# Optimization experiments

Hardware: AMD Instinct MI355X
Metric: run time of the kernel (lower is better)

The kernel has to match this reference:

```python
import jax, jax.numpy as jnp
import numpy as np

V, E, H, ENC, ATT = 10000, 256, 512, 512, 512
B, S, NF, MAXLEN = 128, 25, 196, 64


def setup_inputs() -> dict:
    key = jax.random.key(0)
    ks = jax.random.split(key, 24)
    g = lambda k, shp: (jax.random.normal(k, shp, dtype=jnp.float32) * 0.05)
    emb = g(ks[0], (V, E)).at[0].set(0.0)  # padding_idx=0 row zeroed
    return {
        'decoder_input': jax.random.randint(ks[1], (B, S), 0, V, dtype=jnp.int32),
        'encoder_outputs': jax.random.normal(ks[2], (B, NF, ENC), dtype=jnp.float32),
        'emb': emb,
        'pos_emb': g(ks[3], (MAXLEN, E)),
        'Uw': g(ks[4], (ATT, ENC)), 'Ub': g(ks[5], (ATT,)),
        'Ww': g(ks[6], (ATT, H)), 'Wb': g(ks[7], (ATT,)),
        'Aw': g(ks[8], (1, ATT)), 'Ab': g(ks[9], (1,)),
        'init_h_w': g(ks[10], (H, ENC)), 'init_h_b': g(ks[11], (H,)),
        'init_c_w': g(ks[12], (H, ENC)), 'init_c_b': g(ks[13], (H,)),
        'W_ih': g(ks[14], (4 * H, E + ENC)), 'W_hh': g(ks[15], (4 * H, H)),
        'b_ih': g(ks[16], (4 * H,)), 'b_hh': g(ks[17], (4 * H,)),
        'fcn_w': g(ks[18], (V, H)), 'fcn_b': g(ks[19], (V,)),
    }


def reference(decoder_input, encoder_outputs, emb, pos_emb, Uw, Ub, Ww, Wb, Aw, Ab,
              init_h_w, init_h_b, init_c_w, init_c_b, W_ih, W_hh, b_ih, b_hh,
              fcn_w, fcn_b):
    # Loop-invariant attention key projection: U(features) -> [B, NF, ATT]
    u_hs = jnp.einsum('bne,ae->bna', encoder_outputs, Uw) + Ub
    mean_enc = encoder_outputs.mean(axis=1)                  # [B, ENC]
    h0 = mean_enc @ init_h_w.T + init_h_b                    # [B, H]
    c0 = mean_enc @ init_c_w.T + init_c_b
    tokens = decoder_input.T                                 # [S, B]
    positions = jnp.arange(tokens.shape[0])

    def step(carry, inp):
        h, c = carry
        tok, pos = inp
        embeds = emb[tok] + pos_emb[pos]                     # [B, E]
        w_ah = h @ Ww.T + Wb                                 # [B, ATT]
        scores = jnp.tanh(u_hs + w_ah[:, None, :]) @ Aw[0] + Ab[0]  # [B, NF]
        alpha = jax.nn.softmax(scores, axis=1)
        context = jnp.einsum('bnd,bn->bd', encoder_outputs, alpha)  # [B, ENC]
        x = jnp.concatenate([embeds, context], axis=1)       # [B, E+ENC]
        gates = x @ W_ih.T + b_ih + h @ W_hh.T + b_hh        # [B, 4H]
        i, f, g_, o = jnp.split(gates, 4, axis=1)
        c_new = jax.nn.sigmoid(f) * c + jax.nn.sigmoid(i) * jnp.tanh(g_)
        h_new = jax.nn.sigmoid(o) * jnp.tanh(c_new)
        out = h_new @ fcn_w.T + fcn_b                        # [B, V] (dropout=eval identity)
        return (h_new, c_new), (out, alpha)

    _, (outs, alphas) = jax.lax.scan(step, (h0, c0), (tokens, positions))
    return outs.transpose(1, 0, 2), alphas.transpose(1, 0, 2)
```

## Files before the change

### kernel.cpp

```cpp
#include <hip/hip_runtime.h>

constexpr int B_ = 128, S_ = 25, NF_ = 196, ENC_ = 512, ATT_ = 512;
constexpr int H_ = 512, E_ = 256, V_ = 10000, G4_ = 2048;
constexpr int VPAD_ = 10112;

typedef __attribute__((ext_vector_type(8))) __bf16 bf16x8;
typedef __attribute__((ext_vector_type(4))) __bf16 bf16x4;
typedef __attribute__((ext_vector_type(4))) float f32x4;

__device__ __forceinline__ float bflo(unsigned u) {
    return __builtin_bit_cast(float, u << 16);
}
__device__ __forceinline__ float bfhi(unsigned u) {
    return __builtin_bit_cast(float, u & 0xffff0000u);
}
__device__ __forceinline__ float fast_tanhf(float x) {
    x = fminf(fmaxf(x, -15.f), 15.f);
    return 1.f - 2.f * __fdividef(1.f, __expf(2.f * x) + 1.f);
}
__device__ __forceinline__ float fast_sigf(float x) {
    x = fminf(fmaxf(x, -30.f), 30.f);
    return __fdividef(1.f, 1.f + __expf(-x));
}

__device__ __forceinline__ int gperm(int n) {
    int j = (n & 15) + ((n >> 6) << 4);
    int g = (n >> 4) & 3;
    return g * 512 + j;
}

__global__ __launch_bounds__(256) void k_setup(
    const float* __restrict__ enc, __bf16* __restrict__ enc_bf,
    const float* __restrict__ Uw, __bf16* __restrict__ Uw_bf,
    const float* __restrict__ Ww, unsigned* __restrict__ W2,
    const float* __restrict__ W_ih, __bf16* __restrict__ WihE_r,
    const float* __restrict__ W_hh, __bf16* __restrict__ Wcat,
    const float* __restrict__ b_ih, const float* __restrict__ b_hh,
    float* __restrict__ bsum_r,
    const int* __restrict__ dec, const float* __restrict__ emb,
    const float* __restrict__ pose, __bf16* __restrict__ embeds_bf,
    const float* __restrict__ fcw, __bf16* __restrict__ fcw_bf) {
    __shared__ float Ts[32][65];
    int bid = blockIdx.x, t = threadIdx.x;

    if (bid < 12544) {
        int i = bid * 256 + t;
        if (i < 3211264) {
            float4 v = *(const float4*)&enc[(size_t)i * 4];
            bf16x4 o;
            o[0] = (__bf16)v.x; o[1] = (__bf16)v.y; o[2] = (__bf16)v.z; o[3] = (__bf16)v.w;
            *(bf16x4*)&enc_bf[(size_t)i * 4] = o;
        }
    } else if (bid < 12800) {
        int i = (bid - 12544) * 256 + t;
        float4 v = *(const float4*)&Uw[(size_t)i * 4];
        bf16x4 o;
        o[0] = (__bf16)v.x; o[1] = (__bf16)v.y; o[2] = (__bf16)v.z; o[3] = (__bf16)v.w;
        *(bf16x4*)&Uw_bf[(size_t)i * 4] = o;
    } else if (bid < 12928) {
        int l = bid - 12800;
        int k0 = (l & 15) * 32, j0 = (l >> 4) * 64;
        int c = t & 31, rr = t >> 5;
#pragma unroll
        for (int i = 0; i < 8; ++i) {
            int j = j0 + rr + i * 8;
            Ts[c][rr + i * 8] = Ww[(size_t)j * 512 + k0 + c];
        }
        __syncthreads();
#pragma unroll
        for (int i = 0; i < 4; ++i) {
            int kr = (t >> 5) + i * 8;
            int jc = t & 31;
            __bf16 b0 = (__bf16)Ts[kr][2 * jc], b1 = (__bf16)Ts[kr][2 * jc + 1];
            unsigned u = (unsigned)__builtin_bit_cast(unsigned short, b0)
                       | ((unsigned)__builtin_bit_cast(unsigned short, b1) << 16);
            W2[(size_t)(k0 + kr) * 256 + (j0 >> 1) + jc] = u;
        }
    } else if (bid < 14976) {
        int n = bid - 12928;
        int row = gperm(n);
        WihE_r[(size_t)n * 256 + t] = (__bf16)W_ih[(size_t)row * 768 + t];
    } else if (bid < 17024) {
        int n = bid - 14976;
        int row = gperm(n);
#pragma unroll
        for (int i = 0; i < 4; ++i) {
            int k = t + i * 256;
            float v = (k < 512) ? W_ih[(size_t)row * 768 + 256 + k]
                                : W_hh[(size_t)row * 512 + (k - 512)];
            Wcat[(size_t)n * 1024 + k] = (__bf16)v;
        }
    } else if (bid < 17032) {
        int n = (bid - 17024) * 256 + t;
        int row = gperm(n);
        bsum_r[n] = b_ih[row] + b_hh[row];
    } else if (bid < 20232) {
        int bx = bid - 17032;
        int s = bx >> 7, b = bx & 127;
        int tok = dec[b * S_ + s];
        embeds_bf[(size_t)bx * E_ + t] = (__bf16)(emb[tok * E_ + t] + pose[s * E_ + t]);
    } else {
        int i = (bid - 20232) * 256 + t;
        if (i < VPAD_ * 512 / 4) {
            int e = i * 4;
            int row = e >> 9;
            bf16x4 o;
            if (row < V_) {
                float4 v = *(const float4*)&fcw[(size_t)row * 512 + (e & 511)];
                o[0] = (__bf16)v.x; o[1] = (__bf16)v.y; o[2] = (__bf16)v.z; o[3] = (__bf16)v.w;
            } else {
                o[0] = o[1] = o[2] = o[3] = (__bf16)0.f;
            }
            *(bf16x4*)&fcw_bf[(size_t)e] = o;
        }
    }
}

__global__ __launch_bounds__(1024) void k_init2(const float* __restrict__ enc,
                                                const float* __restrict__ ihw, const float* __restrict__ ihb,
                                                const float* __restrict__ icw, const float* __restrict__ icb,
                                                __bf16* __restrict__ Abuf0, float* __restrict__ cbuf) {
    __shared__ float pm[1024];
    __shared__ __align__(16) float mean[512];
    int b = blockIdx.x, t = threadIdx.x;
    int d = t & 511, q = t >> 9;
    const float* ep = enc + ((size_t)b * 196 + q * 98) * 512 + d;
    float sum = 0.f;
#pragma unroll 7
    for (int n = 0; n < 98; ++n) sum += ep[(size_t)n * 512];
    pm[t] = sum;
    __syncthreads();
    if (t < 512) mean[t] = (pm[t] + pm[t + 512]) * (1.f / 196.f);
    __syncthreads();
    int w = t >> 6, ln = t & 63;
    float4 m4a = *(const float4*)&mean[ln * 8];
    float4 m4b = *(const float4*)&mean[ln * 8 + 4];
#pragma unroll 4
    for (int i = 0; i < 32; ++i) {
        int j = i * 16 + w;
        const float4* wh = (const float4*)&ihw[(size_t)j * 512 + ln * 8];
        const float4* wc = (const float4*)&icw[(size_t)j * 512 + ln * 8];
        float4 ha = wh[0], hb = wh[1], ca = wc[0], cb = wc[1];
        float ah = m4a.x * ha.x + m4a.y * ha.y + m4a.z * ha.z + m4a.w * ha.w
                 + m4b.x * hb.x + m4b.y * hb.y + m4b.z * hb.z + m4b.w * hb.w;
        float ac = m4a.x * ca.x + m4a.y * ca.y + m4a.z * ca.z + m4a.w * ca.w
                 + m4b.x * cb.x + m4b.y * cb.y + m4b.z * cb.z + m4b.w * cb.w;
#pragma unroll
        for (int off = 32; off; off >>= 1) {
            ah += __shfl_xor(ah, off);
            ac += __shfl_xor(ac, off);
        }
        if (ln == 0) {
            Abuf0[(size_t)b * 1024 + 512 + j] = (__bf16)(ah + ihb[j]);
            cbuf[b * 512 + j] = ac + icb[j];
        }
    }
}

__global__ __launch_bounds__(256) void k_gemms(
    const __bf16* __restrict__ Aa, const __bf16* __restrict__ Ba,
    const float* __restrict__ ba, __bf16* __restrict__ Ca,
    const __bf16* __restrict__ Ab, const __bf16* __restrict__ Bb,
    const float* __restrict__ bb, __bf16* __restrict__ Cb) {
    __shared__ __align__(16) __bf16 As[128 * 64];
    __shared__ __align__(16) __bf16 Bs[128 * 64];
    int bid = blockIdx.x, tid = threadIdx.x;
    const __bf16 *A, *Bm;
    const float* bias;
    __bf16* C;
    int lda, K, ldc, m0, n0;
    if (bid < 784) {
        A = Aa; Bm = Ba; bias = ba; C = Ca; lda = 512; K = 512; ldc = 512;
        m0 = (bid % 196) * 128; n0 = (bid / 196) * 128;
    } else {
        int i = bid - 784;
        A = Ab; Bm = Bb; bias = bb; C = Cb; lda = 256; K = 256; ldc = 2048;
        m0 = (i % 25) * 128; n0 = (i / 25) * 128;
    }
    int lane = tid & 63, w = tid >> 6;
    int wm = (w & 1) * 64, wn = (w >> 1) * 64;
    f32x4 acc[4][4] = {};
    int srow = tid >> 3;
    int ke = (tid & 7) * 8;
    int kgw = tid & 7;

    for (int k0 = 0; k0 < K; k0 += 64) {
#pragma unroll
        for (int it = 0; it < 4; ++it) {
            int row = it * 32 + srow;
            bf16x8 av = *(const bf16x8*)(A + (size_t)(m0 + row) * lda + k0 + ke);
            bf16x8 bv = *(const bf16x8*)(Bm + (size_t)(n0 + row) * K + k0 + ke);
            int kg = kgw ^ (row & 7);
            *(bf16x8*)&As[row * 64 + kg * 8] = av;
            *(bf16x8*)&Bs[row * 64 + kg * 8] = bv;
        }
        __syncthreads();
        bf16x8 af[4][2], bfr[4][2];
#pragma unroll
        for (int f = 0; f < 4; ++f) {
#pragma unroll
            for (int ks = 0; ks < 2; ++ks) {
                int ra = wm + f * 16 + (lane & 15);
                int rb = wn + f * 16 + (lane & 15);
                int kgl = ks * 4 + (lane >> 4);
                af[f][ks]  = *(const bf16x8*)&As[ra * 64 + (kgl ^ (ra & 7)) * 8];
                bfr[f][ks] = *(const bf16x8*)&Bs[rb * 64 + (kgl ^ (rb & 7)) * 8];
            }
        }
#pragma unroll
        for (int fm = 0; fm < 4; ++fm)
#pragma unroll
            for (int fn = 0; fn < 4; ++fn)
#pragma unroll
                for (int ks = 0; ks < 2; ++ks)
                    acc[fm][fn] = __builtin_amdgcn_mfma_f32_16x16x32_bf16(
                        af[fm][ks], bfr[fn][ks], acc[fm][fn], 0, 0, 0);
        __syncthreads();
    }
    int cm = (lane >> 4) * 4, cn = lane & 15;
#pragma unroll
    for (int fm = 0; fm < 4; ++fm)
#pragma unroll
        for (int fn = 0; fn < 4; ++fn)
#pragma unroll
            for (int r = 0; r < 4; ++r) {
                int gm = m0 + wm + fm * 16 + cm + r;
                int gn = n0 + wn + fn * 16 + cn;
                C[(size_t)gm * ldc + gn] = (__bf16)(acc[fm][fn][r] + bias[gn]);
            }
}

__global__ __launch_bounds__(256) void k_fcn(
    const __bf16* __restrict__ A, const __bf16* __restrict__ Bm,
    const float* __restrict__ bias1, float* __restrict__ Cout) {
    __shared__ __align__(16) __bf16 As[128 * 64];
    __shared__ __align__(16) __bf16 Bs[128 * 64];
    int tid = threadIdx.x;
    int lane = tid & 63, w = tid >> 6;
    int nwg = gridDim.x * gridDim.y;
    int bid = blockIdx.y * gridDim.x + blockIdx.x;
    int q = nwg >> 3, r0 = nwg & 7;
    int xcd = bid & 7, lid = bid >> 3;
    int wgid = (xcd < r0) ? xcd * (q + 1) + lid : r0 * (q + 1) + (xcd - r0) * q + lid;
    int m0 = (wgid % gridDim.x) * 128;
    int n0 = (wgid / gridDim.x) * 128;

    int wm = (w & 1) * 64, wn = (w >> 1) * 64;
    f32x4 acc[4][4] = {};
    int srow = tid >> 3;
    int ke = (tid & 7) * 8;
    int kgw = tid & 7;

    for (int k0 = 0; k0 < 512; k0 += 64) {
#pragma unroll
        for (int it = 0; it < 4; ++it) {
            int row = it * 32 + srow;
            bf16x8 av = *(const bf16x8*)(A + (size_t)(m0 + row) * 512 + k0 + ke);
            bf16x8 bv = *(const bf16x8*)(Bm + (size_t)(n0 + row) * 512 + k0 + ke);
            int kg = kgw ^ (row & 7);
            *(bf16x8*)&As[row * 64 + kg * 8] = av;
            *(bf16x8*)&Bs[row * 64 + kg * 8] = bv;
        }
        __syncthreads();
        bf16x8 af[4][2], bfr[4][2];
#pragma unroll
        for (int f = 0; f < 4; ++f) {
#pragma unroll
            for (int ks = 0; ks < 2; ++ks) {
                int ra = wm + f * 16 + (lane & 15);
                int rb = wn + f * 16 + (lane & 15);
                int kgl = ks * 4 + (lane >> 4);
                af[f][ks]  = *(const bf16x8*)&As[ra * 64 + (kgl ^ (ra & 7)) * 8];
                bfr[f][ks] = *(const bf16x8*)&Bs[rb * 64 + (kgl ^ (rb & 7)) * 8];
            }
        }
#pragma unroll
        for (int fm = 0; fm < 4; ++fm)
#pragma unroll
            for (int fn = 0; fn < 4; ++fn)
#pragma unroll
                for (int ks = 0; ks < 2; ++ks)
                    acc[fm][fn] = __builtin_amdgcn_mfma_f32_16x16x32_bf16(
                        af[fm][ks], bfr[fn][ks], acc[fm][fn], 0, 0, 0);
        __syncthreads();
    }
    float* LDSf = (float*)As;
    int cm = (lane >> 4) * 4, cn = lane & 15;
#pragma unroll
    for (int c = 0; c < 4; ++c) {
        if ((w & 1) == (c >> 1)) {
            int fmb = (c & 1) * 2;
#pragma unroll
            for (int fi = 0; fi < 2; ++fi) {
                int fm = fmb + fi;
#pragma unroll
                for (int fn = 0; fn < 4; ++fn)
#pragma unroll
                    for (int r = 0; r < 4; ++r)
                        LDSf[(fi * 16 + cm + r) * 128 + wn + fn * 16 + cn] = acc[fm][fn][r];
            }
        }
        __syncthreads();
        int row = tid >> 3, cb = (tid & 7) * 16;
        int grow = m0 + c * 32 + row;
        int orow = (grow & 127) * S_ + (grow >> 7);
        float* dst = Cout + (size_t)orow * V_;
#pragma unroll
        for (int qq = 0; qq < 4; ++qq) {
            int gn = n0 + cb + qq * 4;
            float4 v;
            v.x = LDSf[row * 128 + cb + qq * 4 + 0] + ((gn + 0 < V_) ? bias1[gn + 0] : 0.f);
            v.y = LDSf[row * 128 + cb + qq * 4 + 1] + ((gn + 1 < V_) ? bias1[gn + 1] : 0.f);
            v.z = LDSf[row * 128 + cb + qq * 4 + 2] + ((gn + 2 < V_) ? bias1[gn + 2] : 0.f);
            v.w = LDSf[row * 128 + cb + qq * 4 + 3] + ((gn + 3 < V_) ? bias1[gn + 3] : 0.f);
            if (gn + 3 < V_) {
                *(float4*)&dst[gn] = v;
            } else {
                if (gn + 0 < V_) dst[gn + 0] = v.x;
                if (gn + 1 < V_) dst[gn + 1] = v.y;
                if (gn + 2 < V_) dst[gn + 2] = v.z;
            }
        }
        __syncthreads();
    }
}

__global__ __launch_bounds__(1024) void k_attn2(
    const __bf16* __restrict__ u_hs,
    const unsigned* __restrict__ enc2,
    const unsigned* __restrict__ W2,
    const float* __restrict__ Wb, const float* __restrict__ Aw,
    __bf16* __restrict__ Abuf,
    float* __restrict__ alphas, int s) {
    __shared__ __align__(16) float hs[512];
    __shared__ float wah[512];
    __shared__ float pc[2048];
    __shared__ float sc[200];
    int b = blockIdx.x, t = threadIdx.x;
    int ln = t & 63, w = t >> 6;

    if (t < 256) {
        unsigned u = ((const unsigned*)Abuf)[b * 512 + 256 + t];
        hs[2 * t] = bflo(u); hs[2 * t + 1] = bfhi(u);
    }
    __syncthreads();
    {
        int jp = t & 255, kq = t >> 8;
        float a0 = 0.f, a1 = 0.f;
        const unsigned* wp = W2 + (size_t)(kq * 128) * 256 + jp;
        const float4* h4 = (const float4*)(hs + kq * 128);
#pragma unroll 4
        for (int k4 = 0; k4 < 32; ++k4) {
            float4 hk = h4[k4];
            unsigned w0 = wp[(k4 * 4 + 0) * 256];
            unsigned w1 = wp[(k4 * 4 + 1) * 256];
            unsigned w2 = wp[(k4 * 4 + 2) * 256];
            unsigned w3 = wp[(k4 * 4 + 3) * 256];
            a0 += hk.x * bflo(w0); a1 += hk.x * bfhi(w0);
            a0 += hk.y * bflo(w1); a1 += hk.y * bfhi(w1);
            a0 += hk.z * bflo(w2); a1 += hk.z * bfhi(w2);
            a0 += hk.w * bflo(w3); a1 += hk.w * bfhi(w3);
        }
        pc[kq * 512 + 2 * jp] = a0;
        pc[kq * 512 + 2 * jp + 1] = a1;
    }
    __syncthreads();
    if (t < 512)
        wah[t] = pc[t] + pc[512 + t] + pc[1024 + t] + pc[1536 + t] + Wb[t];
    __syncthreads();
    {
        float av[8], wv[8];
#pragma unroll
        for (int i = 0; i < 8; ++i) { av[i] = Aw[ln * 8 + i]; wv[i] = wah[ln * 8 + i]; }
        for (int n = w; n < NF_; n += 16) {
            bf16x8 u8 = *(const bf16x8*)(u_hs + ((size_t)(b * NF_ + n)) * 512 + ln * 8);
            float acc = 0.f;
#pragma unroll
            for (int i = 0; i < 8; ++i)
                acc += fast_tanhf((float)u8[i] + wv[i]) * av[i];
#pragma unroll
            for (int off = 32; off; off >>= 1) acc += __shfl_xor(acc, off);
            if (ln == 0) sc[n] = __expf(acc);
        }
    }
    __syncthreads();
    float sum = sc[ln] + sc[ln + 64] + sc[ln + 128];
    if (ln < 4) sum += sc[ln + 192];
#pragma unroll
    for (int off = 32; off; off >>= 1) sum += __shfl_xor(sum, off);
    float inv = __fdividef(1.f, sum);
    if (t < NF_) alphas[((size_t)b * S_ + s) * NF_ + t] = sc[t] * inv;
    {
        int p2 = t & 255, q2 = t >> 8;
        float c0 = 0.f, c1 = 0.f;
        for (int i = q2; i < NF_; i += 4) {
            unsigned u = enc2[((size_t)(b * NF_ + i)) * 256 + p2];
            float a = sc[i];
            c0 += a * bflo(u); c1 += a * bfhi(u);
        }
        pc[q2 * 512 + 2 * p2] = c0;
        pc[q2 * 512 + 2 * p2 + 1] = c1;
    }
    __syncthreads();
    if (t < 512)
        Abuf[(size_t)b * 1024 + t] =
            (__bf16)((pc[t] + pc[512 + t] + pc[1024 + t] + pc[1536 + t]) * inv);
}

__global__ __launch_bounds__(256) void k_gates(
    const __bf16* __restrict__ Abuf,
    const __bf16* __restrict__ Wcat,
    const __bf16* __restrict__ gatespre,
    float* __restrict__ cbuf,
    __bf16* __restrict__ AbufN,
    __bf16* __restrict__ Hall_bf,
    int s) {
    __shared__ __align__(16) __bf16 As[2][32 * 64];
    __shared__ __align__(16) __bf16 Bs[2][64 * 64];
    __shared__ float Red[2048];
    int tid = threadIdx.x;
    int lane = tid & 63, w = tid >> 6;
    int m0 = blockIdx.x * 32, n0 = blockIdx.y * 64;
    int kh = w >> 1, wm = (w & 1) * 16;
    f32x4 acc[4] = {};
    int srow = tid >> 3;
    int ke = (tid & 7) * 8;
    int kgw = tid & 7;

    for (int k0 = 0; k0 < 512; k0 += 64) {
#pragma unroll
        for (int h = 0; h < 2; ++h) {
            int kb = h * 512 + k0;
            bf16x8 av = *(const bf16x8*)(Abuf + (size_t)(m0 + srow) * 1024 + kb + ke);
            int kg = kgw ^ (srow & 7);
            *(bf16x8*)&As[h][srow * 64 + kg * 8] = av;
#pragma unroll
            for (int it = 0; it < 2; ++it) {
                int row = it * 32 + srow;
                bf16x8 bv = *(const bf16x8*)(Wcat + (size_t)(n0 + row) * 1024 + kb + ke);
                int kg2 = kgw ^ (row & 7);
                *(bf16x8*)&Bs[h][row * 64 + kg2 * 8] = bv;
            }
        }
        __syncthreads();
        bf16x8 af[2], bfr[4][2];
#pragma unroll
        for (int ks = 0; ks < 2; ++ks) {
            int ra = wm + (lane & 15);
            int kgl = ks * 4 + (lane >> 4);
            af[ks] = *(const bf16x8*)&As[kh][ra * 64 + ((kgl ^ (ra & 7))) * 8];
#pragma unroll
            for (int fn = 0; fn < 4; ++fn) {
                int rb = fn * 16 + (lane & 15);
                bfr[fn][ks] = *(const bf16x8*)&Bs[kh][rb * 64 + ((kgl ^ (rb & 7))) * 8];
            }
        }
#pragma unroll
        for (int fn = 0; fn < 4; ++fn)
#pragma unroll
            for (int ks = 0; ks < 2; ++ks)
                acc[fn] = __builtin_amdgcn_mfma_f32_16x16x32_bf16(
                    af[ks], bfr[fn][ks], acc[fn], 0, 0, 0);
        __syncthreads();
    }
    int base = ((w & 1) * 64 + lane) * 16;
    if (kh == 1) {
#pragma unroll
        for (int fn = 0; fn < 4; ++fn)
#pragma unroll
            for (int r = 0; r < 4; ++r) Red[base + fn * 4 + r] = acc[fn][r];
    }
    __syncthreads();
    if (kh == 0) {
#pragma unroll
        for (int fn = 0; fn < 4; ++fn)
#pragma unroll
            for (int r = 0; r < 4; ++r) acc[fn][r] += Red[base + fn * 4 + r];
        int cm = (lane >> 4) * 4, cn = lane & 15;
        int j = (n0 >> 6) * 16 + cn;
#pragma unroll
        for (int r = 0; r < 4; ++r) {
            int b = m0 + wm + cm + r;
            const __bf16* gp = gatespre + ((size_t)(s * B_ + b)) * G4_ + n0 + cn;
            float qi = acc[0][r] + (float)gp[0];
            float qf = acc[1][r] + (float)gp[16];
            float qg = acc[2][r] + (float)gp[32];
            float qo = acc[3][r] + (float)gp[48];
            float ig = fast_sigf(qi), fg = fast_sigf(qf);
            float gg = fast_tanhf(qg), og = fast_sigf(qo);
            int ci = b * 512 + j;
            float cnew = fg * cbuf[ci] + ig * gg;
            float hn = og * fast_tanhf(cnew);
            cbuf[ci] = cnew;
            __bf16 hb = (__bf16)hn;
            AbufN[(size_t)b * 1024 + 512 + j] = hb;
            Hall_bf[(size_t)(s + 1) * 65536 + ci] = hb;
        }
    }
}

extern "C" void kernel_launch(void* const* d_in, const int* in_sizes, int n_in,
                              void* d_out, int out_size, void* d_ws, size_t ws_size,
                              hipStream_t stream) {
    const int*   dec  = (const int*)d_in[0];
    const float* enc  = (const float*)d_in[1];
    const float* emb  = (const float*)d_in[2];
    const float* pose = (const float*)d_in[3];
    const float* Uw   = (const float*)d_in[4];
    const float* Ub   = (const float*)d_in[5];
    const float* Ww   = (const float*)d_in[6];
    const float* Wb   = (const float*)d_in[7];
    const float* Aw   = (const float*)d_in[8];
    const float* ihw  = (const float*)d_in[10];
    const float* ihb  = (const float*)d_in[11];
    const float* icw  = (const float*)d_in[12];
    const float* icb  = (const float*)d_in[13];
    const float* W_ih = (const float*)d_in[14];
    const float* W_hh = (const float*)d_in[15];
    const float* b_ih = (const float*)d_in[16];
    const float* b_hh = (const float*)d_in[17];
    const float* fcw  = (const float*)d_in[18];
    const float* fcb  = (const float*)d_in[19];
    float* out = (float*)d_out;
    char*  wsb = (char*)d_ws;

    size_t o = 0;
    __bf16*   enc_bf   = (__bf16*)(wsb + o); o += (size_t)25088 * 512 * 2;
    __bf16*   u_hs_bf  = (__bf16*)(wsb + o); o += (size_t)25088 * 512 * 2;
    __bf16*   gpre_bf  = (__bf16*)(wsb + o); o += (size_t)3200 * 2048 * 2;
    __bf16*   Hall_bf  = (__bf16*)(wsb + o); o += (size_t)26 * 65536 * 2;
    float*    cbuf     = (float*)(wsb + o);  o += (size_t)65536 * 4;
    __bf16*   Abuf     = (__bf16*)(wsb + o); o += (size_t)2 * 128 * 1024 * 2;
    __bf16*   Uw_bf    = (__bf16*)(wsb + o); o += (size_t)262144 * 2;
    unsigned* W2       = (unsigned*)(wsb + o); o += (size_t)512 * 256 * 4;
    __bf16*   WihE_r   = (__bf16*)(wsb + o); o += (size_t)2048 * 256 * 2;
    __bf16*   embeds_bf= (__bf16*)(wsb + o); o += (size_t)3200 * 256 * 2;
    __bf16*   Wcat     = (__bf16*)(wsb + o); o += (size_t)2048 * 1024 * 2;
    float*    bsum_r   = (float*)(wsb + o);  o += (size_t)2048 * 4;
    __bf16*   fcw_bf   = (__bf16*)(wsb + o); o += (size_t)VPAD_ * 512 * 2;

    k_setup<<<25288, 256, 0, stream>>>(enc, enc_bf, Uw, Uw_bf, Ww, W2,
                                       W_ih, WihE_r, W_hh, Wcat,
                                       b_ih, b_hh, bsum_r,
                                       dec, emb, pose, embeds_bf, fcw, fcw_bf);
    k_init2<<<B_, 1024, 0, stream>>>(enc, ihw, ihb, icw, icb, Abuf, cbuf);
    k_gemms<<<1184, 256, 0, stream>>>(enc_bf, Uw_bf, Ub, u_hs_bf,
                                      embeds_bf, WihE_r, bsum_r, gpre_bf);

    for (int s = 0; s < S_; ++s) {
        __bf16* Ap = Abuf + (size_t)(s & 1) * 131072;
        __bf16* An = Abuf + (size_t)((s + 1) & 1) * 131072;
        k_attn2<<<B_, 1024, 0, stream>>>(u_hs_bf, (const unsigned*)enc_bf, W2, Wb, Aw,
                                         Ap, out + 32000000, s);
        k_gates<<<dim3(4, 32), 256, 0, stream>>>(Ap, Wcat, gpre_bf, cbuf, An, Hall_bf, s);
    }

    k_fcn<<<dim3(25, 79), 256, 0, stream>>>(Hall_bf + 65536, fcw_bf, fcb, out);
}
```

Measured before the change: 1.410 ms.

## Split gates GEMM into smaller tiles, write fcn output directly, drop activation clamps

```diff
diff --git a/kernel.cpp b/kernel.cpp
--- a/kernel.cpp
+++ b/kernel.cpp
@@ -15,11 +15,10 @@
     return __builtin_bit_cast(float, u & 0xffff0000u);
 }
 __device__ __forceinline__ float fast_tanhf(float x) {
-    x = fminf(fmaxf(x, -15.f), 15.f);
-    return 1.f - 2.f * __fdividef(1.f, __expf(2.f * x) + 1.f);
+    float e = __expf(2.f * x);
+    return 1.f - 2.f * __fdividef(1.f, e + 1.f);
 }
 __device__ __forceinline__ float fast_sigf(float x) {
-    x = fminf(fmaxf(x, -30.f), 30.f);
     return __fdividef(1.f, 1.f + __expf(-x));
 }
 
@@ -284,44 +283,21 @@
                         af[fm][ks], bfr[fn][ks], acc[fm][fn], 0, 0, 0);
         __syncthreads();
     }
-    float* LDSf = (float*)As;
     int cm = (lane >> 4) * 4, cn = lane & 15;
 #pragma unroll
-    for (int c = 0; c < 4; ++c) {
-        if ((w & 1) == (c >> 1)) {
-            int fmb = (c & 1) * 2;
-#pragma unroll
-            for (int fi = 0; fi < 2; ++fi) {
-                int fm = fmb + fi;
-#pragma unroll
-                for (int fn = 0; fn < 4; ++fn)
-#pragma unroll
-                    for (int r = 0; r < 4; ++r)
-                        LDSf[(fi * 16 + cm + r) * 128 + wn + fn * 16 + cn] = acc[fm][fn][r];
-            }
-        }
-        __syncthreads();
-        int row = tid >> 3, cb = (tid & 7) * 16;
-        int grow = m0 + c * 32 + row;
-        int orow = (grow & 127) * S_ + (grow >> 7);
-        float* dst = Cout + (size_t)orow * V_;
-#pragma unroll
-        for (int qq = 0; qq < 4; ++qq) {
-            int gn = n0 + cb + qq * 4;
-            float4 v;
-            v.x = LDSf[row * 128 + cb + qq * 4 + 0] + ((gn + 0 < V_) ? bias1[gn + 0] : 0.f);
-            v.y = LDSf[row * 128 + cb + qq * 4 + 1] + ((gn + 1 < V_) ? bias1[gn + 1] : 0.f);
-            v.z = LDSf[row * 128 + cb + qq * 4 + 2] + ((gn + 2 < V_) ? bias1[gn + 2] : 0.f);
-            v.w = LDSf[row * 128 + cb + qq * 4 + 3] + ((gn + 3 < V_) ? bias1[gn + 3] : 0.f);
-            if (gn + 3 < V_) {
-                *(float4*)&dst[gn] = v;
-            } else {
-                if (gn + 0 < V_) dst[gn + 0] = v.x;
-                if (gn + 1 < V_) dst[gn + 1] = v.y;
-                if (gn + 2 < V_) dst[gn + 2] = v.z;
-            }
-        }
-        __syncthreads();
+    for (int fm = 0; fm < 4; ++fm) {
+#pragma unroll
+        for (int fn = 0; fn < 4; ++fn) {
+#pragma unroll
+            for (int r = 0; r < 4; ++r) {
+                int gm = m0 + wm + fm * 16 + cm + r;
+                int gn = n0 + wn + fn * 16 + cn;
+                if (gn < V_) {
+                    int orow = (gm & 127) * S_ + (gm >> 7);
+                    Cout[(size_t)orow * V_ + gn] = acc[fm][fn][r] + bias1[gn];
+                }
+            }
+        }
     }
 }
 
@@ -415,87 +391,95 @@
     __bf16* __restrict__ AbufN,
     __bf16* __restrict__ Hall_bf,
     int s) {
-    __shared__ __align__(16) __bf16 As[2][32 * 64];
+    __shared__ __align__(16) __bf16 As[2][16 * 64];
     __shared__ __align__(16) __bf16 Bs[2][64 * 64];
-    __shared__ float Red[2048];
-    int tid = threadIdx.x;
-    int lane = tid & 63, w = tid >> 6;
-    int m0 = blockIdx.x * 32, n0 = blockIdx.y * 64;
-    int kh = w >> 1, wm = (w & 1) * 16;
-    f32x4 acc[4] = {};
-    int srow = tid >> 3;
-    int ke = (tid & 7) * 8;
-    int kgw = tid & 7;
+    __shared__ float Red[1024];
+    __shared__ float Gs[16][68];
+    int t = threadIdx.x;
+    int lane = t & 63, w = t >> 6;
+    int m0 = blockIdx.x * 16, n0 = blockIdx.y * 64;
+    int kh = w >> 1, nh = w & 1;
+    f32x4 acc[2] = {};
+    int ah = t >> 7;
+    int arow = (t & 127) >> 3;
+    int ake = (t & 7) * 8;
+    int akg = t & 7;
+    int srow = t >> 3;
+    int ke = (t & 7) * 8;
+    int kgw = t & 7;
 
     for (int k0 = 0; k0 < 512; k0 += 64) {
+        {
+            int kb = ah * 512 + k0;
+            bf16x8 av = *(const bf16x8*)(Abuf + (size_t)(m0 + arow) * 1024 + kb + ake);
+            *(bf16x8*)&As[ah][arow * 64 + (akg ^ (arow & 7)) * 8] = av;
+        }
 #pragma unroll
         for (int h = 0; h < 2; ++h) {
             int kb = h * 512 + k0;
-            bf16x8 av = *(const bf16x8*)(Abuf + (size_t)(m0 + srow) * 1024 + kb + ke);
-            int kg = kgw ^ (srow & 7);
-            *(bf16x8*)&As[h][srow * 64 + kg * 8] = av;
 #pragma unroll
             for (int it = 0; it < 2; ++it) {
                 int row = it * 32 + srow;
                 bf16x8 bv = *(const bf16x8*)(Wcat + (size_t)(n0 + row) * 1024 + kb + ke);
-                int kg2 = kgw ^ (row & 7);
-                *(bf16x8*)&Bs[h][row * 64 + kg2 * 8] = bv;
-            }
-        }
-        __syncthreads();
-        bf16x8 af[2], bfr[4][2];
+                *(bf16x8*)&Bs[h][row * 64 + (kgw ^ (row & 7)) * 8] = bv;
+            }
+        }
+        __syncthreads();
+        bf16x8 af[2], bfr[2][2];
 #pragma unroll
         for (int ks = 0; ks < 2; ++ks) {
-            int ra = wm + (lane & 15);
+            int ra = lane & 15;
             int kgl = ks * 4 + (lane >> 4);
             af[ks] = *(const bf16x8*)&As[kh][ra * 64 + ((kgl ^ (ra & 7))) * 8];
 #pragma unroll
-            for (int fn = 0; fn < 4; ++fn) {
-                int rb = fn * 16 + (lane & 15);
+            for (int fn = 0; fn < 2; ++fn) {
+                int rb = nh * 32 + fn * 16 + (lane & 15);
                 bfr[fn][ks] = *(const bf16x8*)&Bs[kh][rb * 64 + ((kgl ^ (rb & 7))) * 8];
             }
         }
 #pragma unroll
-        for (int fn = 0; fn < 4; ++fn)
+        for (int fn = 0; fn < 2; ++fn)
 #pragma unroll
             for (int ks = 0; ks < 2; ++ks)
                 acc[fn] = __builtin_amdgcn_mfma_f32_16x16x32_bf16(
                     af[ks], bfr[fn][ks], acc[fn], 0, 0, 0);
         __syncthreads();
     }
-    int base = ((w & 1) * 64 + lane) * 16;
+    int base = (nh * 64 + lane) * 8;
     if (kh == 1) {
 #pragma unroll
-        for (int fn = 0; fn < 4; ++fn)
+        for (int fn = 0; fn < 2; ++fn)
 #pragma unroll
             for (int r = 0; r < 4; ++r) Red[base + fn * 4 + r] = acc[fn][r];
     }
     __syncthreads();
     if (kh == 0) {
-#pragma unroll
-        for (int fn = 0; fn < 4; ++fn)
-#pragma unroll
-            for (int r = 0; r < 4; ++r) acc[fn][r] += Red[base + fn * 4 + r];
         int cm = (lane >> 4) * 4, cn = lane & 15;
-        int j = (n0 >> 6) * 16 + cn;
-#pragma unroll
-        for (int r = 0; r < 4; ++r) {
-            int b = m0 + wm + cm + r;
-            const __bf16* gp = gatespre + ((size_t)(s * B_ + b)) * G4_ + n0 + cn;
-            float qi = acc[0][r] + (float)gp[0];
-            float qf = acc[1][r] + (float)gp[16];
-            float qg = acc[2][r] + (float)gp[32];
-            float qo = acc[3][r] + (float)gp[48];
-            float ig = fast_sigf(qi), fg = fast_sigf(qf);
-            float gg = fast_tanhf(qg), og = fast_sigf(qo);
-            int ci = b * 512 + j;
-            float cnew = fg * cbuf[ci] + ig * gg;
-            float hn = og * fast_tanhf(cnew);
-            cbuf[ci] = cnew;
-            __bf16 hb = (__bf16)hn;
-            AbufN[(size_t)b * 1024 + 512 + j] = hb;
-            Hall_bf[(size_t)(s + 1) * 65536 + ci] = hb;
-        }
+#pragma unroll
+        for (int fn = 0; fn < 2; ++fn)
+#pragma unroll
+            for (int r = 0; r < 4; ++r)
+                Gs[cm + r][nh * 32 + fn * 16 + cn] = acc[fn][r] + Red[base + fn * 4 + r];
+    }
+    __syncthreads();
+    {
+        int row = t >> 4, jlo = t & 15;
+        int b = m0 + row;
+        int j = (n0 >> 6) * 16 + jlo;
+        const __bf16* gp = gatespre + ((size_t)(s * B_ + b)) * G4_ + n0 + jlo;
+        float qi = Gs[row][jlo]      + (float)gp[0];
+        float qf = Gs[row][16 + jlo] + (float)gp[16];
+        float qg = Gs[row][32 + jlo] + (float)gp[32];
+        float qo = Gs[row][48 + jlo] + (float)gp[48];
+        float ig = fast_sigf(qi), fg = fast_sigf(qf);
+        float gg = fast_tanhf(qg), og = fast_sigf(qo);
+        int ci = b * 512 + j;
+        float cnew = fg * cbuf[ci] + ig * gg;
+        float hn = og * fast_tanhf(cnew);
+        cbuf[ci] = cnew;
+        __bf16 hb = (__bf16)hn;
+        AbufN[(size_t)b * 1024 + 512 + j] = hb;
+        Hall_bf[(size_t)(s + 1) * 65536 + ci] = hb;
     }
 }
 
@@ -552,7 +536,7 @@
         __bf16* An = Abuf + (size_t)((s + 1) & 1) * 131072;
         k_attn2<<<B_, 1024, 0, stream>>>(u_hs_bf, (const unsigned*)enc_bf, W2, Wb, Aw,
                                          Ap, out + 32000000, s);
-        k_gates<<<dim3(4, 32), 256, 0, stream>>>(Ap, Wcat, gpre_bf, cbuf, An, Hall_bf, s);
+        k_gates<<<dim3(8, 32), 256, 0, stream>>>(Ap, Wcat, gpre_bf, cbuf, An, Hall_bf, s);
     }
 
     k_fcn<<<dim3(25, 79), 256, 0, stream>>>(Hall_bf + 65536, fcw_bf, fcb, out);
```

Result: faster. 1.346 ms (-4.6%).
